# Performance work log

Hardware: AMD Instinct MI355X
Metric: run time of the kernel (lower is better)

## Reference

```python
import jax, jax.numpy as jnp
import numpy as np

B, T_D, T_P = 64, 256, 1024
DRUG_DIM, PROT_DIM, D = 128, 128, 128
MAX_LEN = 1024
NEG = -1e9


def _linear_params(k, out_d, in_d):
    k1, k2 = jax.random.split(k)
    lim = 1.0 / np.sqrt(in_d)
    W = jax.random.uniform(k1, (out_d, in_d), minval=-lim, maxval=lim, dtype=jnp.float32)
    b = jax.random.uniform(k2, (out_d,), minval=-lim, maxval=lim, dtype=jnp.float32)
    return W, b


def setup_inputs() -> dict:
    key = jax.random.key(0)
    ks = jax.random.split(key, 13)
    inp = {
        'smiles_embeddings': jax.random.normal(ks[0], (B, T_D, DRUG_DIM), dtype=jnp.float32),
        'protein_embeddings': jax.random.normal(ks[1], (B, T_P, PROT_DIM), dtype=jnp.float32),
        'smiles_mask': jax.random.randint(ks[2], (B, T_D), 0, 2, dtype=jnp.int32),
        'protein_mask': jax.random.randint(ks[3], (B, T_P), 0, 2, dtype=jnp.int32),
        # torch inits pos_bias to zeros; small random values make the test nontrivial
        'pos_bias': 0.02 * jax.random.normal(ks[4], (MAX_LEN, MAX_LEN), dtype=jnp.float32),
    }
    names = [('Wqd', 'bqd', DRUG_DIM), ('Wkp', 'bkp', PROT_DIM), ('Wvp', 'bvp', PROT_DIM),
             ('Wqp', 'bqp', PROT_DIM), ('Wkd', 'bkd', DRUG_DIM), ('Wvd', 'bvd', DRUG_DIM),
             ('Wpd', 'bpd', D), ('Wpp', 'bpp', D)]
    for i, (wn, bn, in_d) in enumerate(names):
        W, b = _linear_params(ks[5 + i], D, in_d)
        inp[wn] = W
        inp[bn] = b
    return inp


def _lin(x, W, b):
    return x @ W.T + b


def _aft(q, k, v, pb_masked, Wp, bp):
    # q: [B,Ti,D]; k,v: [B,Tj,D]; pb_masked: [B,Ti,Tj]
    max_k = k.max(axis=1, keepdims=True)              # per (b,d) over seq j
    max_pb = pb_masked.max(axis=2, keepdims=True)     # per (b,i) over j
    exp_k = jnp.exp(k - max_k)                        # [B,Tj,D]
    exp_pb = jnp.exp(pb_masked - max_pb)              # [B,Ti,Tj]
    num = jnp.einsum('bij,bjd->bid', exp_pb, exp_k * v)
    den = jnp.einsum('bij,bjd->bid', exp_pb, exp_k)
    y = jax.nn.sigmoid(q) * num / den
    return _lin(y, Wp, bp)


def reference(smiles_embeddings, protein_embeddings, smiles_mask, protein_mask, pos_bias,
              Wqd, bqd, Wkp, bkp, Wvp, bvp, Wqp, bqp, Wkd, bkd, Wvd, bvd, Wpd, bpd, Wpp, bpp):
    Td = smiles_embeddings.shape[1]
    Tp = protein_embeddings.shape[1]
    combined = smiles_mask[:, :, None] * protein_mask[:, None, :]  # [B,Td,Tp]
    pb = pos_bias[:Td, :Tp][None]                                   # [1,Td,Tp]

    # drug queries attend over protein keys/values
    pb_d = jnp.where(combined == 0, NEG, pb)
    y_d = _aft(_lin(smiles_embeddings, Wqd, bqd),
               _lin(protein_embeddings, Wkp, bkp),
               _lin(protein_embeddings, Wvp, bvp), pb_d, Wpd, bpd)

    # protein queries attend over drug keys/values (transposed pos bias)
    pb_p = jnp.where(jnp.swapaxes(combined, 1, 2) == 0, NEG, jnp.swapaxes(pb, 1, 2))
    y_p = _aft(_lin(protein_embeddings, Wqp, bqp),
               _lin(smiles_embeddings, Wkd, bkd),
               _lin(smiles_embeddings, Wvd, bvd), pb_p, Wpp, bpp)

    y_d = jnp.where(smiles_mask[:, :, None] == 0, NEG, y_d).max(axis=1)   # [B,D]
    y_p = jnp.where(protein_mask[:, :, None] == 0, NEG, y_p).max(axis=1)  # [B,D]
    return y_d, y_p
```

## Files before the change

kernel.cpp:

```cpp
#include <hip/hip_runtime.h>
#include <cstdint>
#include <cstddef>

#define NEGV -1e9f

typedef __bf16 bf16x8 __attribute__((ext_vector_type(8)));
typedef float f32x4 __attribute__((ext_vector_type(4)));
typedef unsigned short us4 __attribute__((ext_vector_type(4)));
typedef unsigned short us8 __attribute__((ext_vector_type(8)));

__device__ __forceinline__ unsigned short f2bf(float f) {
  unsigned int u = __float_as_uint(f);
  u += 0x7fffu + ((u >> 16) & 1u);
  return (unsigned short)(u >> 16);
}
__device__ __forceinline__ float bf2f(unsigned short u) {
  return __uint_as_float(((unsigned)u) << 16);
}


__global__ void prep_kernel(const float* __restrict__ w0, const float* __restrict__ w1,
                            const float* __restrict__ w2, const float* __restrict__ w3,
                            const float* __restrict__ w4, const float* __restrict__ w5,
                            const float* __restrict__ w6, const float* __restrict__ w7,
                            unsigned short* __restrict__ Wbf,
                            const float* __restrict__ pb,
                            unsigned short* __restrict__ epb,
                            unsigned short* __restrict__ epbT,
                            unsigned int* __restrict__ outEnc) {
  __shared__ unsigned short t[32][33];
  const int blk = blockIdx.x, tid = threadIdx.x;
  if (blk < 64) {
    outEnc[blk * 256 + tid] = 0u;
    return;
  }
  if (blk < 192) {
    const float* Ws[8] = {w0, w1, w2, w3, w4, w5, w6, w7};
    int idx = (blk - 64) * 256 + tid;
    int mat = idx >> 12, off = idx & 4095;
    float4 v = *(const float4*)&Ws[mat][(size_t)off * 4];
    us4 p;
    p.x = f2bf(v.x); p.y = f2bf(v.y); p.z = f2bf(v.z); p.w = f2bf(v.w);
    *(us4*)&Wbf[(size_t)mat * 16384 + (size_t)off * 4] = p;
    return;
  }
  const int bid = blk - 192;
  const int j0 = (bid & 31) * 32, i0 = (bid >> 5) * 32;
  const int tx = tid & 31, ty = tid >> 5;
#pragma unroll
  for (int r = 0; r < 4; ++r) {
    int i = i0 + ty + r * 8;
    unsigned short u = f2bf(__expf(pb[(size_t)i * 1024 + j0 + tx]));
    epb[(size_t)i * 1024 + j0 + tx] = u;
    t[ty + r * 8][tx] = u;
  }
  __syncthreads();
#pragma unroll
  for (int r = 0; r < 4; ++r)
    epbT[(size_t)(j0 + ty + r * 8) * 256 + i0 + tx] = t[tx][ty + r * 8];
}

__global__ __launch_bounds__(256) void proj3_all(
    const float* __restrict__ smiles, const float* __restrict__ prot,
    const int* __restrict__ smask, const int* __restrict__ pmask,
    const unsigned short* __restrict__ Wbf,
    const float* __restrict__ bqd, const float* __restrict__ bkd, const float* __restrict__ bvd,
    const float* __restrict__ bqp, const float* __restrict__ bkp, const float* __restrict__ bvp,
    const unsigned short* __restrict__ epb, const unsigned short* __restrict__ epbT,
    unsigned short* __restrict__ AFd, unsigned short* __restrict__ AFp,
    unsigned short* __restrict__ SQd, unsigned short* __restrict__ BKd,
    unsigned short* __restrict__ BVd,
    unsigned short* __restrict__ SQp, unsigned short* __restrict__ BKp,
    unsigned short* __restrict__ BVp) {
  const int tid = threadIdx.x;

  if (blockIdx.x >= 1280) {
    int sid = (blockIdx.x - 1280) * 256 + tid;
    if (sid < 32768) {
      int lane = sid & 63, kt = (sid >> 6) & 31, it = sid >> 11;
      int i = it * 16 + (lane & 15), j = kt * 32 + (lane >> 4) * 8;
      *(us8*)&AFd[(size_t)sid * 8] = *(const us8*)&epb[(size_t)i * 1024 + j];
    } else {
      int s2 = sid - 32768;
      int lane = s2 & 63, kt = (s2 >> 6) & 7, it = s2 >> 9;
      int i = it * 16 + (lane & 15), j = kt * 32 + (lane >> 4) * 8;
      *(us8*)&AFp[(size_t)s2 * 8] = *(const us8*)&epbT[(size_t)i * 256 + j];
    }
    return;
  }

  __shared__ unsigned short xL[64 * 136];

  const float* X; const int* mask;
  const unsigned short *Wq, *Wk, *Wv;
  const float *bq, *bk_, *bv;
  unsigned short *SQ, *BK, *BV;
  int T, g0;
  if (blockIdx.x < 256) {
    X = smiles; mask = smask; T = 256; g0 = blockIdx.x * 64;
    Wq = Wbf; Wk = Wbf + 16384; Wv = Wbf + 32768;
    bq = bqd; bk_ = bkd; bv = bvd;
    SQ = SQd; BK = BKd; BV = BVd;
  } else {
    X = prot; mask = pmask; T = 1024; g0 = (blockIdx.x - 256) * 64;
    Wq = Wbf + 3 * 16384; Wk = Wbf + 4 * 16384; Wv = Wbf + 5 * 16384;
    bq = bqp; bk_ = bkp; bv = bvp;
    SQ = SQp; BK = BKp; BV = BVp;
  }
  const int b = g0 / T;
  const int tl0 = g0 - b * T;
  const int NIT = T / 16, NKT = T / 32;

#pragma unroll
  for (int r = 0; r < 8; ++r) {
    int i4 = tid + 256 * r;
    int t = i4 >> 5, k4 = (i4 & 31) * 4;
    float4 v = *(const float4*)&X[(size_t)(g0 + t) * 128 + k4];
    us4 p;
    p.x = f2bf(v.x); p.y = f2bf(v.y); p.z = f2bf(v.z); p.w = f2bf(v.w);
    *(us4*)&xL[t * 136 + k4] = p;
  }
  __syncthreads();

  const int lane = tid & 63, wave = tid >> 6;
  const int lo = lane & 15, hi = lane >> 4;
  const int d0 = wave * 32;

  f32x4 aQ[4][2], aK[4][2], aV[4][2];
#pragma unroll
  for (int a = 0; a < 4; ++a)
#pragma unroll
    for (int s = 0; s < 2; ++s)
#pragma unroll
      for (int r = 0; r < 4; ++r) { aQ[a][s][r] = 0.f; aK[a][s][r] = 0.f; aV[a][s][r] = 0.f; }

#pragma unroll
  for (int kt = 0; kt < 128; kt += 32) {
    bf16x8 bQ[2], bK[2], bV[2];
#pragma unroll
    for (int s = 0; s < 2; ++s) {
      size_t roff = (size_t)(d0 + s * 16 + lo) * 128 + kt + hi * 8;
      bQ[s] = *(const bf16x8*)&Wq[roff];
      bK[s] = *(const bf16x8*)&Wk[roff];
      bV[s] = *(const bf16x8*)&Wv[roff];
    }
#pragma unroll
    for (int a = 0; a < 4; ++a) {
      bf16x8 af = *(const bf16x8*)&xL[(a * 16 + lo) * 136 + kt + hi * 8];
#pragma unroll
      for (int s = 0; s < 2; ++s) {
        aQ[a][s] = __builtin_amdgcn_mfma_f32_16x16x32_bf16(af, bQ[s], aQ[a][s], 0, 0, 0);
        aK[a][s] = __builtin_amdgcn_mfma_f32_16x16x32_bf16(af, bK[s], aK[a][s], 0, 0, 0);
        aV[a][s] = __builtin_amdgcn_mfma_f32_16x16x32_bf16(af, bV[s], aV[a][s], 0, 0, 0);
      }
    }
  }

#pragma unroll
  for (int s = 0; s < 2; ++s) {
    int dt = (d0 >> 4) + s;
    float bb = bq[d0 + s * 16 + lo];
#pragma unroll
    for (int a = 0; a < 4; ++a) {
      int it = (tl0 >> 4) + a;
      us4 v;
#pragma unroll
      for (int r = 0; r < 4; ++r) {
        float q = aQ[a][s][r] + bb;
        v[r] = f2bf(1.f / (1.f + __expf(-q)));
      }
      ((us4*)SQ)[(((size_t)b * NIT + it) * 8 + dt) * 64 + lane] = v;
    }
  }

#pragma unroll
  for (int s = 0; s < 2; ++s) {
    int dt = (d0 >> 4) + s;
    float bbk = bk_[d0 + s * 16 + lo], bbv = bv[d0 + s * 16 + lo];
#pragma unroll
    for (int a = 0; a < 4; ++a) {
      int kt = (tl0 >> 5) + (a >> 1);
      int lane_f = ((a & 1) * 2 + (hi >> 1)) * 16 + lo;
      us4 vk, vv;
#pragma unroll
      for (int r = 0; r < 4; ++r) {
        int tg = g0 + a * 16 + hi * 4 + r;
        int mk = mask[tg];
        float ek = mk ? __expf(aK[a][s][r] + bbk) : 0.f;
        float ekv = ek * (aV[a][s][r] + bbv);
        vk[r] = f2bf(ek);
        vv[r] = f2bf(ekv);
      }
      size_t q4 = ((((size_t)b * NKT + kt) * 8 + dt) * 64 + lane_f) * 2 + (hi & 1);
      ((us4*)BK)[q4] = vk;
      ((us4*)BV)[q4] = vv;
    }
  }
}

__global__ __launch_bounds__(256, 2) void aft_all(
    const unsigned short* __restrict__ AFd, const unsigned short* __restrict__ AFp,
    const unsigned short* __restrict__ SQd, const unsigned short* __restrict__ BKd,
    const unsigned short* __restrict__ BVd,
    const unsigned short* __restrict__ SQp, const unsigned short* __restrict__ BKp,
    const unsigned short* __restrict__ BVp,
    const int* __restrict__ smask, const int* __restrict__ pmask,
    const unsigned short* __restrict__ Wbf,
    const float* __restrict__ bpd, const float* __restrict__ bpp,
    unsigned int* __restrict__ outEnc) {
  __shared__ unsigned short yL[128 * 136];

  const int blk = blockIdx.x;
  const unsigned short *AF, *BK, *BV, *SQ, *Wp;
  const float* bp;
  const int* msk;
  unsigned int* oEnc;
  int b, i0, NKT, NIT;
  if (blk < 128) {
    b = blk & 63; i0 = (blk >> 6) * 128; NKT = 32; NIT = 16;
    AF = AFd; BK = BKp; BV = BVp; SQ = SQd;
    Wp = Wbf + 6 * 16384; bp = bpd; msk = smask + b * 256 + i0; oEnc = outEnc;
  } else {
    int k = blk - 128;
    b = k & 63; i0 = (k >> 6) * 128; NKT = 8; NIT = 64;
    AF = AFp; BK = BKd; BV = BVd; SQ = SQp;
    Wp = Wbf + 7 * 16384; bp = bpp; msk = pmask + b * 1024 + i0; oEnc = outEnc + 8192;
  }

  const int tid = threadIdx.x, lane = tid & 63, w = tid >> 6;
  const int lo = lane & 15, hi = lane >> 4;
  const int wi = (w >> 1) * 64, wd = (w & 1) * 64;
  const int it0 = (i0 + wi) >> 4;
  const int dt0 = wd >> 4;

  const unsigned short* BKb = BK + (size_t)b * NKT * 8 * 64 * 8;
  const unsigned short* BVb = BV + (size_t)b * NKT * 8 * 64 * 8;

  f32x4 aN[4][4], aD[4][4];
#pragma unroll
  for (int a = 0; a < 4; ++a)
#pragma unroll
    for (int n = 0; n < 4; ++n)
#pragma unroll
      for (int r = 0; r < 4; ++r) { aN[a][n][r] = 0.f; aD[a][n][r] = 0.f; }

#pragma unroll 2
  for (int kt = 0; kt < NKT; ++kt) {
    bf16x8 af[4];
#pragma unroll
    for (int a = 0; a < 4; ++a)
      af[a] = *(const bf16x8*)&AF[(((size_t)(it0 + a) * NKT + kt) * 64 + lane) * 8];
    bf16x8 bk[4], bv[4];
#pragma unroll
    for (int n = 0; n < 4; ++n) {
      size_t x = (((size_t)kt * 8 + dt0 + n) * 64 + lane) * 8;
      bk[n] = *(const bf16x8*)&BKb[x];
      bv[n] = *(const bf16x8*)&BVb[x];
    }
#pragma unroll
    for (int a = 0; a < 4; ++a)
#pragma unroll
      for (int n = 0; n < 4; ++n) {
        aN[a][n] = __builtin_amdgcn_mfma_f32_16x16x32_bf16(af[a], bv[n], aN[a][n], 0, 0, 0);
        aD[a][n] = __builtin_amdgcn_mfma_f32_16x16x32_bf16(af[a], bk[n], aD[a][n], 0, 0, 0);
      }
  }

#pragma unroll
  for (int a = 0; a < 4; ++a)
#pragma unroll
    for (int n = 0; n < 4; ++n) {
      us4 q = ((const us4*)SQ)[(((size_t)b * NIT + it0 + a) * 8 + dt0 + n) * 64 + lane];
      int iL = wi + a * 16 + hi * 4;
      int d = wd + n * 16 + lo;
#pragma unroll
      for (int r = 0; r < 4; ++r) {
        float y = bf2f(q[r]) * __fdividef(aN[a][n][r], aD[a][n][r]);
        yL[(iL + r) * 136 + d] = f2bf(y);
      }
    }
  __syncthreads();

  f32x4 aZ[4][4];
#pragma unroll
  for (int a = 0; a < 4; ++a)
#pragma unroll
    for (int n = 0; n < 4; ++n)
#pragma unroll
      for (int r = 0; r < 4; ++r) aZ[a][n][r] = 0.f;

#pragma unroll
  for (int kt = 0; kt < 128; kt += 32) {
    bf16x8 bw[4];
#pragma unroll
    for (int n = 0; n < 4; ++n)
      bw[n] = *(const bf16x8*)&Wp[(size_t)(wd + n * 16 + lo) * 128 + kt + hi * 8];
#pragma unroll
    for (int a = 0; a < 4; ++a) {
      bf16x8 af = *(const bf16x8*)&yL[(wi + a * 16 + lo) * 136 + kt + hi * 8];
#pragma unroll
      for (int n = 0; n < 4; ++n)
        aZ[a][n] = __builtin_amdgcn_mfma_f32_16x16x32_bf16(af, bw[n], aZ[a][n], 0, 0, 0);
    }
  }

#pragma unroll
  for (int n = 0; n < 4; ++n) {
    int d = wd + n * 16 + lo;
    float bb = bp[d];
    float m = NEGV;
#pragma unroll
    for (int a = 0; a < 4; ++a)
#pragma unroll
      for (int r = 0; r < 4; ++r) {
        int iL = wi + a * 16 + hi * 4 + r;
        float z = aZ[a][n][r] + bb;
        m = msk[iL] ? fmaxf(m, z) : m;
      }
    m = fmaxf(m, __shfl_xor(m, 16, 64));
    m = fmaxf(m, __shfl_xor(m, 32, 64));
    if (hi == 0) {
      unsigned bits = __float_as_uint(m);
      unsigned key = (bits & 0x80000000u) ? ~bits : (bits | 0x80000000u);
      atomicMax(&oEnc[b * 128 + d], key);
    }
  }
}

__global__ void out_decode(unsigned int* o) {
  int i = blockIdx.x * 256 + threadIdx.x;
  unsigned k = o[i];
  unsigned bits = (k & 0x80000000u) ? (k ^ 0x80000000u) : ~k;
  ((float*)o)[i] = __uint_as_float(bits);
}

extern "C" void kernel_launch(void* const* d_in, const int* in_sizes, int n_in,
                              void* d_out, int out_size, void* d_ws, size_t ws_size,
                              hipStream_t stream) {
  const float* smiles = (const float*)d_in[0];
  const float* prot   = (const float*)d_in[1];
  const int* smask = (const int*)d_in[2];
  const int* pmask = (const int*)d_in[3];
  const float* pos_bias = (const float*)d_in[4];
  const float* Wqd = (const float*)d_in[5];  const float* bqd = (const float*)d_in[6];
  const float* Wkp = (const float*)d_in[7];  const float* bkp = (const float*)d_in[8];
  const float* Wvp = (const float*)d_in[9];  const float* bvp = (const float*)d_in[10];
  const float* Wqp = (const float*)d_in[11]; const float* bqp = (const float*)d_in[12];
  const float* Wkd = (const float*)d_in[13]; const float* bkd = (const float*)d_in[14];
  const float* Wvd = (const float*)d_in[15]; const float* bvd = (const float*)d_in[16];
  const float* Wpd = (const float*)d_in[17]; const float* bpd = (const float*)d_in[18];
  const float* Wpp = (const float*)d_in[19]; const float* bpp = (const float*)d_in[20];

  unsigned short* u = (unsigned short*)d_ws;
  unsigned short* BKp_  = u;
  unsigned short* BVp_  = BKp_ + 8388608;
  unsigned short* BKd_  = BVp_ + 8388608;
  unsigned short* BVd_  = BKd_ + 2097152;
  unsigned short* SQd_  = BVd_ + 2097152;
  unsigned short* SQp_  = SQd_ + 2097152;
  unsigned short* epb_  = SQp_ + 8388608;
  unsigned short* epbT_ = epb_ + 262144;
  unsigned short* AFd_  = epbT_ + 262144;
  unsigned short* AFp_  = AFd_ + 262144;
  unsigned short* Wbf   = AFp_ + 262144;

  dim3 blk(256);

  prep_kernel<<<448, blk, 0, stream>>>(Wqd, Wkd, Wvd, Wqp, Wkp, Wvp, Wpd, Wpp,
                                       Wbf, pos_bias, epb_, epbT_,
                                       (unsigned int*)d_out);

  proj3_all<<<1536, blk, 0, stream>>>(smiles, prot, smask, pmask, Wbf,
                                      bqd, bkd, bvd, bqp, bkp, bvp,
                                      epb_, epbT_, AFd_, AFp_,
                                      SQd_, BKd_, BVd_, SQp_, BKp_, BVp_);

  aft_all<<<640, blk, 0, stream>>>(AFd_, AFp_, SQd_, BKd_, BVd_,
                                   SQp_, BKp_, BVp_, smask, pmask, Wbf,
                                   bpd, bpp, (unsigned int*)d_out);

  out_decode<<<64, blk, 0, stream>>>((unsigned int*)d_out);
}
```

Baseline: 181.6 us.

## Split projection and AFT numerator/denominator work across doubled waves per block

Both proj3_all and aft_all move to 512-thread blocks. In proj3_all, four waves compute K/V and four compute Q. In aft_all, half the waves accumulate the numerator and half the denominator. The denominator is passed through LDS in bf16 so the numerator waves can form y, and the output projection is redistributed over all eight waves. The aim is to halve per-wave accumulator registers and raise occupancy and parallelism, at the cost of an extra LDS round-trip, an extra barrier, and bf16 rounding of the denominator.

```diff
diff --git a/kernel.cpp b/kernel.cpp
--- a/kernel.cpp
+++ b/kernel.cpp
@@ -60,7 +60,7 @@
     epbT[(size_t)(j0 + ty + r * 8) * 256 + i0 + tx] = t[tx][ty + r * 8];
 }
 
-__global__ __launch_bounds__(256) void proj3_all(
+__global__ __launch_bounds__(512, 4) void proj3_all(
     const float* __restrict__ smiles, const float* __restrict__ prot,
     const int* __restrict__ smask, const int* __restrict__ pmask,
     const unsigned short* __restrict__ Wbf,
@@ -75,7 +75,7 @@
   const int tid = threadIdx.x;
 
   if (blockIdx.x >= 1280) {
-    int sid = (blockIdx.x - 1280) * 256 + tid;
+    int sid = (blockIdx.x - 1280) * 512 + tid;
     if (sid < 32768) {
       int lane = sid & 63, kt = (sid >> 6) & 31, it = sid >> 11;
       int i = it * 16 + (lane & 15), j = kt * 32 + (lane >> 4) * 8;
@@ -112,8 +112,8 @@
   const int NIT = T / 16, NKT = T / 32;
 
 #pragma unroll
-  for (int r = 0; r < 8; ++r) {
-    int i4 = tid + 256 * r;
+  for (int r = 0; r < 4; ++r) {
+    int i4 = tid + 512 * r;
     int t = i4 >> 5, k4 = (i4 & 31) * 4;
     float4 v = *(const float4*)&X[(size_t)(g0 + t) * 128 + k4];
     us4 p;
@@ -124,81 +124,107 @@
 
   const int lane = tid & 63, wave = tid >> 6;
   const int lo = lane & 15, hi = lane >> 4;
-  const int d0 = wave * 32;
-
-  f32x4 aQ[4][2], aK[4][2], aV[4][2];
-#pragma unroll
-  for (int a = 0; a < 4; ++a)
-#pragma unroll
-    for (int s = 0; s < 2; ++s)
-#pragma unroll
-      for (int r = 0; r < 4; ++r) { aQ[a][s][r] = 0.f; aK[a][s][r] = 0.f; aV[a][s][r] = 0.f; }
-
-#pragma unroll
-  for (int kt = 0; kt < 128; kt += 32) {
-    bf16x8 bQ[2], bK[2], bV[2];
+
+  if (wave < 4) {
+    const int d0 = wave * 32;
+    f32x4 aK[4][2], aV[4][2];
+#pragma unroll
+    for (int a = 0; a < 4; ++a)
+#pragma unroll
+      for (int s = 0; s < 2; ++s)
+#pragma unroll
+        for (int r = 0; r < 4; ++r) { aK[a][s][r] = 0.f; aV[a][s][r] = 0.f; }
+
+#pragma unroll
+    for (int kt = 0; kt < 128; kt += 32) {
+      bf16x8 bK[2], bV[2];
+#pragma unroll
+      for (int s = 0; s < 2; ++s) {
+        size_t roff = (size_t)(d0 + s * 16 + lo) * 128 + kt + hi * 8;
+        bK[s] = *(const bf16x8*)&Wk[roff];
+        bV[s] = *(const bf16x8*)&Wv[roff];
+      }
+#pragma unroll
+      for (int a = 0; a < 4; ++a) {
+        bf16x8 af = *(const bf16x8*)&xL[(a * 16 + lo) * 136 + kt + hi * 8];
+#pragma unroll
+        for (int s = 0; s < 2; ++s) {
+          aK[a][s] = __builtin_amdgcn_mfma_f32_16x16x32_bf16(af, bK[s], aK[a][s], 0, 0, 0);
+          aV[a][s] = __builtin_amdgcn_mfma_f32_16x16x32_bf16(af, bV[s], aV[a][s], 0, 0, 0);
+        }
+      }
+    }
+
 #pragma unroll
     for (int s = 0; s < 2; ++s) {
-      size_t roff = (size_t)(d0 + s * 16 + lo) * 128 + kt + hi * 8;
-      bQ[s] = *(const bf16x8*)&Wq[roff];
-      bK[s] = *(const bf16x8*)&Wk[roff];
-      bV[s] = *(const bf16x8*)&Wv[roff];
-    }
-#pragma unroll
-    for (int a = 0; a < 4; ++a) {
-      bf16x8 af = *(const bf16x8*)&xL[(a * 16 + lo) * 136 + kt + hi * 8];
+      int dt = (d0 >> 4) + s;
+      float bbk = bk_[d0 + s * 16 + lo], bbv = bv[d0 + s * 16 + lo];
+#pragma unroll
+      for (int a = 0; a < 4; ++a) {
+        int kt = (tl0 >> 5) + (a >> 1);
+        int lane_f = ((a & 1) * 2 + (hi >> 1)) * 16 + lo;
+        us4 vk, vv;
+#pragma unroll
+        for (int r = 0; r < 4; ++r) {
+          int tg = g0 + a * 16 + hi * 4 + r;
+          int mk = mask[tg];
+          float ek = mk ? __expf(aK[a][s][r] + bbk) : 0.f;
+          float ekv = ek * (aV[a][s][r] + bbv);
+          vk[r] = f2bf(ek);
+          vv[r] = f2bf(ekv);
+        }
+        size_t q4 = ((((size_t)b * NKT + kt) * 8 + dt) * 64 + lane_f) * 2 + (hi & 1);
+        ((us4*)BK)[q4] = vk;
+        ((us4*)BV)[q4] = vv;
+      }
+    }
+  } else {
+    const int d0 = (wave - 4) * 32;
+    f32x4 aQ[4][2];
+#pragma unroll
+    for (int a = 0; a < 4; ++a)
+#pragma unroll
+      for (int s = 0; s < 2; ++s)
+#pragma unroll
+        for (int r = 0; r < 4; ++r) aQ[a][s][r] = 0.f;
+
+#pragma unroll
+    for (int kt = 0; kt < 128; kt += 32) {
+      bf16x8 bQ[2];
 #pragma unroll
       for (int s = 0; s < 2; ++s) {
-        aQ[a][s] = __builtin_amdgcn_mfma_f32_16x16x32_bf16(af, bQ[s], aQ[a][s], 0, 0, 0);
-        aK[a][s] = __builtin_amdgcn_mfma_f32_16x16x32_bf16(af, bK[s], aK[a][s], 0, 0, 0);
-        aV[a][s] = __builtin_amdgcn_mfma_f32_16x16x32_bf16(af, bV[s], aV[a][s], 0, 0, 0);
-      }
-    }
-  }
-
-#pragma unroll
-  for (int s = 0; s < 2; ++s) {
-    int dt = (d0 >> 4) + s;
-    float bb = bq[d0 + s * 16 + lo];
-#pragma unroll
-    for (int a = 0; a < 4; ++a) {
-      int it = (tl0 >> 4) + a;
-      us4 v;
-#pragma unroll
-      for (int r = 0; r < 4; ++r) {
-        float q = aQ[a][s][r] + bb;
-        v[r] = f2bf(1.f / (1.f + __expf(-q)));
-      }
-      ((us4*)SQ)[(((size_t)b * NIT + it) * 8 + dt) * 64 + lane] = v;
-    }
-  }
-
-#pragma unroll
-  for (int s = 0; s < 2; ++s) {
-    int dt = (d0 >> 4) + s;
-    float bbk = bk_[d0 + s * 16 + lo], bbv = bv[d0 + s * 16 + lo];
-#pragma unroll
-    for (int a = 0; a < 4; ++a) {
-      int kt = (tl0 >> 5) + (a >> 1);
-      int lane_f = ((a & 1) * 2 + (hi >> 1)) * 16 + lo;
-      us4 vk, vv;
-#pragma unroll
-      for (int r = 0; r < 4; ++r) {
-        int tg = g0 + a * 16 + hi * 4 + r;
-        int mk = mask[tg];
-        float ek = mk ? __expf(aK[a][s][r] + bbk) : 0.f;
-        float ekv = ek * (aV[a][s][r] + bbv);
-        vk[r] = f2bf(ek);
-        vv[r] = f2bf(ekv);
-      }
-      size_t q4 = ((((size_t)b * NKT + kt) * 8 + dt) * 64 + lane_f) * 2 + (hi & 1);
-      ((us4*)BK)[q4] = vk;
-      ((us4*)BV)[q4] = vv;
-    }
-  }
-}
-
-__global__ __launch_bounds__(256, 2) void aft_all(
+        size_t roff = (size_t)(d0 + s * 16 + lo) * 128 + kt + hi * 8;
+        bQ[s] = *(const bf16x8*)&Wq[roff];
+      }
+#pragma unroll
+      for (int a = 0; a < 4; ++a) {
+        bf16x8 af = *(const bf16x8*)&xL[(a * 16 + lo) * 136 + kt + hi * 8];
+#pragma unroll
+        for (int s = 0; s < 2; ++s)
+          aQ[a][s] = __builtin_amdgcn_mfma_f32_16x16x32_bf16(af, bQ[s], aQ[a][s], 0, 0, 0);
+      }
+    }
+
+#pragma unroll
+    for (int s = 0; s < 2; ++s) {
+      int dt = (d0 >> 4) + s;
+      float bb = bq[d0 + s * 16 + lo];
+#pragma unroll
+      for (int a = 0; a < 4; ++a) {
+        int it = (tl0 >> 4) + a;
+        us4 v;
+#pragma unroll
+        for (int r = 0; r < 4; ++r) {
+          float q = aQ[a][s][r] + bb;
+          v[r] = f2bf(1.f / (1.f + __expf(-q)));
+        }
+        ((us4*)SQ)[(((size_t)b * NIT + it) * 8 + dt) * 64 + lane] = v;
+      }
+    }
+  }
+}
+
+__global__ __launch_bounds__(512, 4) void aft_all(
     const unsigned short* __restrict__ AFd, const unsigned short* __restrict__ AFp,
     const unsigned short* __restrict__ SQd, const unsigned short* __restrict__ BKd,
     const unsigned short* __restrict__ BVd,
@@ -208,7 +234,9 @@
     const unsigned short* __restrict__ Wbf,
     const float* __restrict__ bpd, const float* __restrict__ bpp,
     unsigned int* __restrict__ outEnc) {
-  __shared__ unsigned short yL[128 * 136];
+  __shared__ unsigned short smem[16384 + 128 * 136];
+  unsigned short* denL = smem;
+  unsigned short* yL = smem + 16384;
 
   const int blk = blockIdx.x;
   const unsigned short *AF, *BK, *BV, *SQ, *Wp;
@@ -229,20 +257,20 @@
 
   const int tid = threadIdx.x, lane = tid & 63, w = tid >> 6;
   const int lo = lane & 15, hi = lane >> 4;
-  const int wi = (w >> 1) * 64, wd = (w & 1) * 64;
+  const int wv = w & 3;
+  const int wi = (wv >> 1) * 64, wd = (wv & 1) * 64;
   const int it0 = (i0 + wi) >> 4;
   const int dt0 = wd >> 4;
 
-  const unsigned short* BKb = BK + (size_t)b * NKT * 8 * 64 * 8;
-  const unsigned short* BVb = BV + (size_t)b * NKT * 8 * 64 * 8;
-
-  f32x4 aN[4][4], aD[4][4];
+  const unsigned short* Bb = ((w < 4) ? BV : BK) + (size_t)b * NKT * 8 * 64 * 8;
+
+  f32x4 acc[4][4];
 #pragma unroll
   for (int a = 0; a < 4; ++a)
 #pragma unroll
     for (int n = 0; n < 4; ++n)
 #pragma unroll
-      for (int r = 0; r < 4; ++r) { aN[a][n][r] = 0.f; aD[a][n][r] = 0.f; }
+      for (int r = 0; r < 4; ++r) acc[a][n][r] = 0.f;
 
 #pragma unroll 2
   for (int kt = 0; kt < NKT; ++kt) {
@@ -250,40 +278,52 @@
 #pragma unroll
     for (int a = 0; a < 4; ++a)
       af[a] = *(const bf16x8*)&AF[(((size_t)(it0 + a) * NKT + kt) * 64 + lane) * 8];
-    bf16x8 bk[4], bv[4];
-#pragma unroll
-    for (int n = 0; n < 4; ++n) {
-      size_t x = (((size_t)kt * 8 + dt0 + n) * 64 + lane) * 8;
-      bk[n] = *(const bf16x8*)&BKb[x];
-      bv[n] = *(const bf16x8*)&BVb[x];
-    }
+    bf16x8 bb[4];
+#pragma unroll
+    for (int n = 0; n < 4; ++n)
+      bb[n] = *(const bf16x8*)&Bb[(((size_t)kt * 8 + dt0 + n) * 64 + lane) * 8];
+#pragma unroll
+    for (int a = 0; a < 4; ++a)
+#pragma unroll
+      for (int n = 0; n < 4; ++n)
+        acc[a][n] = __builtin_amdgcn_mfma_f32_16x16x32_bf16(af[a], bb[n], acc[a][n], 0, 0, 0);
+  }
+
+  if (w >= 4) {
 #pragma unroll
     for (int a = 0; a < 4; ++a)
 #pragma unroll
       for (int n = 0; n < 4; ++n) {
-        aN[a][n] = __builtin_amdgcn_mfma_f32_16x16x32_bf16(af[a], bv[n], aN[a][n], 0, 0, 0);
-        aD[a][n] = __builtin_amdgcn_mfma_f32_16x16x32_bf16(af[a], bk[n], aD[a][n], 0, 0, 0);
-      }
-  }
-
-#pragma unroll
-  for (int a = 0; a < 4; ++a)
-#pragma unroll
-    for (int n = 0; n < 4; ++n) {
-      us4 q = ((const us4*)SQ)[(((size_t)b * NIT + it0 + a) * 8 + dt0 + n) * 64 + lane];
-      int iL = wi + a * 16 + hi * 4;
-      int d = wd + n * 16 + lo;
-#pragma unroll
-      for (int r = 0; r < 4; ++r) {
-        float y = bf2f(q[r]) * __fdividef(aN[a][n][r], aD[a][n][r]);
-        yL[(iL + r) * 136 + d] = f2bf(y);
-      }
-    }
+        us4 v;
+#pragma unroll
+        for (int r = 0; r < 4; ++r) v[r] = f2bf(acc[a][n][r]);
+        ((us4*)denL)[(wv * 16 + a * 4 + n) * 64 + lane] = v;
+      }
+  }
   __syncthreads();
 
-  f32x4 aZ[4][4];
-#pragma unroll
-  for (int a = 0; a < 4; ++a)
+  if (w < 4) {
+#pragma unroll
+    for (int a = 0; a < 4; ++a)
+#pragma unroll
+      for (int n = 0; n < 4; ++n) {
+        us4 dv = ((const us4*)denL)[(wv * 16 + a * 4 + n) * 64 + lane];
+        us4 q = ((const us4*)SQ)[(((size_t)b * NIT + it0 + a) * 8 + dt0 + n) * 64 + lane];
+        int iL = wi + a * 16 + hi * 4;
+        int d = wd + n * 16 + lo;
+#pragma unroll
+        for (int r = 0; r < 4; ++r) {
+          float y = bf2f(q[r]) * __fdividef(acc[a][n][r], bf2f(dv[r]));
+          yL[(iL + r) * 136 + d] = f2bf(y);
+        }
+      }
+  }
+  __syncthreads();
+
+  const int wi2 = (w & 3) * 32, wd2 = (w >> 2) * 64;
+  f32x4 aZ[2][4];
+#pragma unroll
+  for (int a = 0; a < 2; ++a)
 #pragma unroll
     for (int n = 0; n < 4; ++n)
 #pragma unroll
@@ -294,10 +334,10 @@
     bf16x8 bw[4];
 #pragma unroll
     for (int n = 0; n < 4; ++n)
-      bw[n] = *(const bf16x8*)&Wp[(size_t)(wd + n * 16 + lo) * 128 + kt + hi * 8];
-#pragma unroll
-    for (int a = 0; a < 4; ++a) {
-      bf16x8 af = *(const bf16x8*)&yL[(wi + a * 16 + lo) * 136 + kt + hi * 8];
+      bw[n] = *(const bf16x8*)&Wp[(size_t)(wd2 + n * 16 + lo) * 128 + kt + hi * 8];
+#pragma unroll
+    for (int a = 0; a < 2; ++a) {
+      bf16x8 af = *(const bf16x8*)&yL[(wi2 + a * 16 + lo) * 136 + kt + hi * 8];
 #pragma unroll
       for (int n = 0; n < 4; ++n)
         aZ[a][n] = __builtin_amdgcn_mfma_f32_16x16x32_bf16(af, bw[n], aZ[a][n], 0, 0, 0);
@@ -306,14 +346,14 @@
 
 #pragma unroll
   for (int n = 0; n < 4; ++n) {
-    int d = wd + n * 16 + lo;
+    int d = wd2 + n * 16 + lo;
     float bb = bp[d];
     float m = NEGV;
 #pragma unroll
-    for (int a = 0; a < 4; ++a)
+    for (int a = 0; a < 2; ++a)
 #pragma unroll
       for (int r = 0; r < 4; ++r) {
-        int iL = wi + a * 16 + hi * 4 + r;
+        int iL = wi2 + a * 16 + hi * 4 + r;
         float z = aZ[a][n][r] + bb;
         m = msk[iL] ? fmaxf(m, z) : m;
       }
@@ -364,20 +404,18 @@
   unsigned short* AFp_  = AFd_ + 262144;
   unsigned short* Wbf   = AFp_ + 262144;
 
-  dim3 blk(256);
-
-  prep_kernel<<<448, blk, 0, stream>>>(Wqd, Wkd, Wvd, Wqp, Wkp, Wvp, Wpd, Wpp,
+  prep_kernel<<<448, 256, 0, stream>>>(Wqd, Wkd, Wvd, Wqp, Wkp, Wvp, Wpd, Wpp,
                                        Wbf, pos_bias, epb_, epbT_,
                                        (unsigned int*)d_out);
 
-  proj3_all<<<1536, blk, 0, stream>>>(smiles, prot, smask, pmask, Wbf,
+  proj3_all<<<1408, 512, 0, stream>>>(smiles, prot, smask, pmask, Wbf,
                                       bqd, bkd, bvd, bqp, bkp, bvp,
                                       epb_, epbT_, AFd_, AFp_,
                                       SQd_, BKd_, BVd_, SQp_, BKp_, BVp_);
 
-  aft_all<<<640, blk, 0, stream>>>(AFd_, AFp_, SQd_, BKd_, BVd_,
+  aft_all<<<640, 512, 0, stream>>>(AFd_, AFp_, SQd_, BKd_, BVd_,
                                    SQp_, BKp_, BVp_, smask, pmask, Wbf,
                                    bpd, bpp, (unsigned int*)d_out);
 
-  out_decode<<<64, blk, 0, stream>>>((unsigned int*)d_out);
-}
+  out_decode<<<64, 256, 0, stream>>>((unsigned int*)d_out);
+}
```

After: 190.1 us. +4.7%, slower.

## Split AFT numerator/denominator across waves with halved row tiles and register prefetch

Applied to the files above, without the earlier changes.

The attention kernel now processes 64 query rows per block instead of 128, doubling the grid. Within a block, half the waves compute the numerator and half the denominator, exchanging the denominator through LDS as bf16. This halves per-wave accumulator registers so occupancy can be raised. The main loop also software-prefetches the next k-tile into registers, and the output projection is re-tiled so each wave owns 16 rows across all 128 columns. The cost is an extra LDS round trip and barrier, duplicated A-fragment loads across waves, and bf16 rounding of the denominator.

```diff
diff --git a/kernel.cpp b/kernel.cpp
--- a/kernel.cpp
+++ b/kernel.cpp
@@ -198,7 +198,7 @@
   }
 }
 
-__global__ __launch_bounds__(256, 2) void aft_all(
+__global__ __launch_bounds__(256, 3) void aft_all(
     const unsigned short* __restrict__ AFd, const unsigned short* __restrict__ AFp,
     const unsigned short* __restrict__ SQd, const unsigned short* __restrict__ BKd,
     const unsigned short* __restrict__ BVd,
@@ -208,7 +208,9 @@
     const unsigned short* __restrict__ Wbf,
     const float* __restrict__ bpd, const float* __restrict__ bpp,
     unsigned int* __restrict__ outEnc) {
-  __shared__ unsigned short yL[128 * 136];
+  __shared__ unsigned short smem[8192 + 64 * 136];
+  unsigned short* denL = smem;
+  unsigned short* yL = smem + 8192;
 
   const int blk = blockIdx.x;
   const unsigned short *AF, *BK, *BV, *SQ, *Wp;
@@ -216,107 +218,121 @@
   const int* msk;
   unsigned int* oEnc;
   int b, i0, NKT, NIT;
-  if (blk < 128) {
-    b = blk & 63; i0 = (blk >> 6) * 128; NKT = 32; NIT = 16;
+  if (blk < 256) {
+    b = blk & 63; i0 = (blk >> 6) * 64; NKT = 32; NIT = 16;
     AF = AFd; BK = BKp; BV = BVp; SQ = SQd;
     Wp = Wbf + 6 * 16384; bp = bpd; msk = smask + b * 256 + i0; oEnc = outEnc;
   } else {
-    int k = blk - 128;
-    b = k & 63; i0 = (k >> 6) * 128; NKT = 8; NIT = 64;
+    int k = blk - 256;
+    b = k & 63; i0 = (k >> 6) * 64; NKT = 8; NIT = 64;
     AF = AFp; BK = BKd; BV = BVd; SQ = SQp;
     Wp = Wbf + 7 * 16384; bp = bpp; msk = pmask + b * 1024 + i0; oEnc = outEnc + 8192;
   }
 
   const int tid = threadIdx.x, lane = tid & 63, w = tid >> 6;
   const int lo = lane & 15, hi = lane >> 4;
-  const int wi = (w >> 1) * 64, wd = (w & 1) * 64;
-  const int it0 = (i0 + wi) >> 4;
-  const int dt0 = wd >> 4;
-
-  const unsigned short* BKb = BK + (size_t)b * NKT * 8 * 64 * 8;
-  const unsigned short* BVb = BV + (size_t)b * NKT * 8 * 64 * 8;
-
-  f32x4 aN[4][4], aD[4][4];
+  const int h = w & 1;
+  const int isden = w >> 1;
+  const int it0 = i0 >> 4;
+  const int dt0 = h * 4;
+
+  const unsigned short* Bb = (isden ? BK : BV) + (size_t)b * NKT * 8 * 64 * 8;
+
+  f32x4 acc[4][4];
 #pragma unroll
   for (int a = 0; a < 4; ++a)
 #pragma unroll
     for (int n = 0; n < 4; ++n)
 #pragma unroll
-      for (int r = 0; r < 4; ++r) { aN[a][n][r] = 0.f; aD[a][n][r] = 0.f; }
-
-#pragma unroll 2
+      for (int r = 0; r < 4; ++r) acc[a][n][r] = 0.f;
+
+  bf16x8 af[4], bb[4];
+#pragma unroll
+  for (int a = 0; a < 4; ++a)
+    af[a] = *(const bf16x8*)&AF[(((size_t)(it0 + a) * NKT + 0) * 64 + lane) * 8];
+#pragma unroll
+  for (int n = 0; n < 4; ++n)
+    bb[n] = *(const bf16x8*)&Bb[(((size_t)0 * 8 + dt0 + n) * 64 + lane) * 8];
+
   for (int kt = 0; kt < NKT; ++kt) {
-    bf16x8 af[4];
+    const int k2 = (kt + 1 < NKT) ? kt + 1 : kt;
+    bf16x8 afn[4], bbn[4];
 #pragma unroll
     for (int a = 0; a < 4; ++a)
-      af[a] = *(const bf16x8*)&AF[(((size_t)(it0 + a) * NKT + kt) * 64 + lane) * 8];
-    bf16x8 bk[4], bv[4];
-#pragma unroll
-    for (int n = 0; n < 4; ++n) {
-      size_t x = (((size_t)kt * 8 + dt0 + n) * 64 + lane) * 8;
-      bk[n] = *(const bf16x8*)&BKb[x];
-      bv[n] = *(const bf16x8*)&BVb[x];
-    }
+      afn[a] = *(const bf16x8*)&AF[(((size_t)(it0 + a) * NKT + k2) * 64 + lane) * 8];
+#pragma unroll
+    for (int n = 0; n < 4; ++n)
+      bbn[n] = *(const bf16x8*)&Bb[(((size_t)k2 * 8 + dt0 + n) * 64 + lane) * 8];
 #pragma unroll
     for (int a = 0; a < 4; ++a)
 #pragma unroll
+      for (int n = 0; n < 4; ++n)
+        acc[a][n] = __builtin_amdgcn_mfma_f32_16x16x32_bf16(af[a], bb[n], acc[a][n], 0, 0, 0);
+#pragma unroll
+    for (int a = 0; a < 4; ++a) af[a] = afn[a];
+#pragma unroll
+    for (int n = 0; n < 4; ++n) bb[n] = bbn[n];
+  }
+
+  if (isden) {
+#pragma unroll
+    for (int a = 0; a < 4; ++a)
+#pragma unroll
       for (int n = 0; n < 4; ++n) {
-        aN[a][n] = __builtin_amdgcn_mfma_f32_16x16x32_bf16(af[a], bv[n], aN[a][n], 0, 0, 0);
-        aD[a][n] = __builtin_amdgcn_mfma_f32_16x16x32_bf16(af[a], bk[n], aD[a][n], 0, 0, 0);
-      }
-  }
-
-#pragma unroll
-  for (int a = 0; a < 4; ++a)
-#pragma unroll
-    for (int n = 0; n < 4; ++n) {
-      us4 q = ((const us4*)SQ)[(((size_t)b * NIT + it0 + a) * 8 + dt0 + n) * 64 + lane];
-      int iL = wi + a * 16 + hi * 4;
-      int d = wd + n * 16 + lo;
-#pragma unroll
-      for (int r = 0; r < 4; ++r) {
-        float y = bf2f(q[r]) * __fdividef(aN[a][n][r], aD[a][n][r]);
-        yL[(iL + r) * 136 + d] = f2bf(y);
-      }
-    }
+        us4 v;
+#pragma unroll
+        for (int r = 0; r < 4; ++r) v[r] = f2bf(acc[a][n][r]);
+        ((us4*)denL)[((h * 4 + a) * 4 + n) * 64 + lane] = v;
+      }
+  }
   __syncthreads();
 
-  f32x4 aZ[4][4];
-#pragma unroll
-  for (int a = 0; a < 4; ++a)
-#pragma unroll
-    for (int n = 0; n < 4; ++n)
-#pragma unroll
-      for (int r = 0; r < 4; ++r) aZ[a][n][r] = 0.f;
+  if (!isden) {
+#pragma unroll
+    for (int a = 0; a < 4; ++a)
+#pragma unroll
+      for (int n = 0; n < 4; ++n) {
+        us4 dv = ((const us4*)denL)[((h * 4 + a) * 4 + n) * 64 + lane];
+        us4 q = ((const us4*)SQ)[(((size_t)b * NIT + it0 + a) * 8 + dt0 + n) * 64 + lane];
+        int iL = a * 16 + hi * 4;
+        int d = h * 64 + n * 16 + lo;
+#pragma unroll
+        for (int r = 0; r < 4; ++r) {
+          float y = bf2f(q[r]) * __fdividef(acc[a][n][r], bf2f(dv[r]));
+          yL[(iL + r) * 136 + d] = f2bf(y);
+        }
+      }
+  }
+  __syncthreads();
+
+  const int wi2 = w * 16;
+  f32x4 aZ[8];
+#pragma unroll
+  for (int n = 0; n < 8; ++n)
+#pragma unroll
+    for (int r = 0; r < 4; ++r) aZ[n][r] = 0.f;
 
 #pragma unroll
   for (int kt = 0; kt < 128; kt += 32) {
-    bf16x8 bw[4];
-#pragma unroll
-    for (int n = 0; n < 4; ++n)
-      bw[n] = *(const bf16x8*)&Wp[(size_t)(wd + n * 16 + lo) * 128 + kt + hi * 8];
-#pragma unroll
-    for (int a = 0; a < 4; ++a) {
-      bf16x8 af = *(const bf16x8*)&yL[(wi + a * 16 + lo) * 136 + kt + hi * 8];
-#pragma unroll
-      for (int n = 0; n < 4; ++n)
-        aZ[a][n] = __builtin_amdgcn_mfma_f32_16x16x32_bf16(af, bw[n], aZ[a][n], 0, 0, 0);
-    }
-  }
-
-#pragma unroll
-  for (int n = 0; n < 4; ++n) {
-    int d = wd + n * 16 + lo;
-    float bb = bp[d];
+    bf16x8 af2 = *(const bf16x8*)&yL[(wi2 + lo) * 136 + kt + hi * 8];
+#pragma unroll
+    for (int n = 0; n < 8; ++n) {
+      bf16x8 bw = *(const bf16x8*)&Wp[(size_t)(n * 16 + lo) * 128 + kt + hi * 8];
+      aZ[n] = __builtin_amdgcn_mfma_f32_16x16x32_bf16(af2, bw, aZ[n], 0, 0, 0);
+    }
+  }
+
+#pragma unroll
+  for (int n = 0; n < 8; ++n) {
+    int d = n * 16 + lo;
+    float bbia = bp[d];
     float m = NEGV;
 #pragma unroll
-    for (int a = 0; a < 4; ++a)
-#pragma unroll
-      for (int r = 0; r < 4; ++r) {
-        int iL = wi + a * 16 + hi * 4 + r;
-        float z = aZ[a][n][r] + bb;
-        m = msk[iL] ? fmaxf(m, z) : m;
-      }
+    for (int r = 0; r < 4; ++r) {
+      int iL = wi2 + hi * 4 + r;
+      float z = aZ[n][r] + bbia;
+      m = msk[iL] ? fmaxf(m, z) : m;
+    }
     m = fmaxf(m, __shfl_xor(m, 16, 64));
     m = fmaxf(m, __shfl_xor(m, 32, 64));
     if (hi == 0) {
@@ -364,20 +380,18 @@
   unsigned short* AFp_  = AFd_ + 262144;
   unsigned short* Wbf   = AFp_ + 262144;
 
-  dim3 blk(256);
-
-  prep_kernel<<<448, blk, 0, stream>>>(Wqd, Wkd, Wvd, Wqp, Wkp, Wvp, Wpd, Wpp,
+  prep_kernel<<<448, 256, 0, stream>>>(Wqd, Wkd, Wvd, Wqp, Wkp, Wvp, Wpd, Wpp,
                                        Wbf, pos_bias, epb_, epbT_,
                                        (unsigned int*)d_out);
 
-  proj3_all<<<1536, blk, 0, stream>>>(smiles, prot, smask, pmask, Wbf,
+  proj3_all<<<1536, 256, 0, stream>>>(smiles, prot, smask, pmask, Wbf,
                                       bqd, bkd, bvd, bqp, bkp, bvp,
                                       epb_, epbT_, AFd_, AFp_,
                                       SQd_, BKd_, BVd_, SQp_, BKp_, BVp_);
 
-  aft_all<<<640, blk, 0, stream>>>(AFd_, AFp_, SQd_, BKd_, BVd_,
-                                   SQp_, BKp_, BVp_, smask, pmask, Wbf,
-                                   bpd, bpp, (unsigned int*)d_out);
-
-  out_decode<<<64, blk, 0, stream>>>((unsigned int*)d_out);
-}
+  aft_all<<<1280, 256, 0, stream>>>(AFd_, AFp_, SQd_, BKd_, BVd_,
+                                    SQp_, BKp_, BVp_, smask, pmask, Wbf,
+                                    bpd, bpp, (unsigned int*)d_out);
+
+  out_decode<<<64, 256, 0, stream>>>((unsigned int*)d_out);
+}
```

Result: slower. 190.5 us (+4.9%).
